# Performance work log

Hardware: AMD Instinct MI355X
Metric: run time of the kernel (lower is better)

Reference implementation:

```python
import jax, jax.numpy as jnp
import numpy as np

NUM_STAGES = 3
EPS = 1e-6


def _l2norm(x, axis):
    return x / (EPS + jnp.linalg.norm(x, axis=axis, keepdims=True))


def _l1norm(x, axis):
    return x / (EPS + jnp.sum(x, axis=axis, keepdims=True))


def setup_inputs() -> dict:
    key = jax.random.key(0)
    k1, k2 = jax.random.split(key)
    B, C, H, W, K = 16, 512, 64, 64, 64
    feats = jax.random.normal(k1, (B, C, H, W), dtype=jnp.float32)
    # bases buffer: N(0, sqrt(2/K)) then l2-normalized along channel dim (done in reference)
    bases = jax.random.normal(k2, (1, C, K), dtype=jnp.float32) * np.sqrt(2.0 / K)
    return {"feats": feats, "bases": bases}


def reference(feats, bases):
    B, C, H, W = feats.shape
    f = feats.reshape(B, C, H * W)              # [B, C, N]
    b = _l2norm(bases, axis=1)                  # match buffer init normalization
    b = jnp.broadcast_to(b, (B, C, b.shape[2])) # [B, C, K]
    attention = None
    for _ in range(NUM_STAGES):
        attention = jnp.einsum('bcn,bck->bnk', f, b)        # [B, N, K]
        attention = jax.nn.softmax(attention, axis=2)
        attention_normed = _l1norm(attention, axis=1)
        b = jnp.einsum('bcn,bnk->bck', f, attention_normed)  # [B, C, K]
        b = _l2norm(b, axis=1)
    # EM loop runs under torch.no_grad in the original
    b = jax.lax.stop_gradient(b)
    attention = jax.lax.stop_gradient(attention)
    feats_recon = jnp.einsum('bck,bnk->bcn', b, attention)   # [B, C, N]
    return feats_recon.reshape(B, C, H, W)
```

## Files before the change

kernel.cpp:

```cpp
#include <hip/hip_runtime.h>
#include <stdint.h>

#define B_ 16
#define C_ 512
#define N_ 4096
#define K_ 64
#define NUM_STAGES 3

typedef __bf16 bf16x8 __attribute__((ext_vector_type(8)));
typedef float f32x4 __attribute__((ext_vector_type(4)));

__device__ __forceinline__ uint16_t f2bf(float x) {
  union { float f; uint32_t u; } v; v.f = x;
  uint32_t r = (v.u + 0x7FFFu + ((v.u >> 16) & 1u)) >> 16;
  return (uint16_t)r;
}

__device__ __forceinline__ void async16(const uint16_t* g, uint16_t* l) {
  __builtin_amdgcn_global_load_lds(
      (const __attribute__((address_space(1))) unsigned int*)g,
      (__attribute__((address_space(3))) unsigned int*)l, 16, 0, 0);
}

__global__ __launch_bounds__(256) void k_prep(const float* __restrict__ feats,
                                              uint16_t* __restrict__ f16,
                                              uint16_t* __restrict__ fT16) {
  __shared__ uint16_t tile[64][65];
  int b = blockIdx.z, c0 = blockIdx.y * 64, n0 = blockIdx.x * 64;
  int t = threadIdx.x;
  const float* src = feats + ((size_t)b * C_ + c0) * N_ + n0;
  uint16_t* dst = f16 + ((size_t)b * C_ + c0) * N_ + n0;
  int cl = t >> 4;
  int nl = (t & 15) * 4;
#pragma unroll
  for (int i = 0; i < 4; ++i) {
    int c = cl + 16 * i;
    float4 v = *(const float4*)(src + (size_t)c * N_ + nl);
    ushort4 x;
    x.x = f2bf(v.x); x.y = f2bf(v.y); x.z = f2bf(v.z); x.w = f2bf(v.w);
    *(ushort4*)(dst + (size_t)c * N_ + nl) = x;
    tile[c][nl + 0] = x.x; tile[c][nl + 1] = x.y;
    tile[c][nl + 2] = x.z; tile[c][nl + 3] = x.w;
  }
  __syncthreads();
  uint16_t* dstT = fT16 + ((size_t)b * N_ + n0) * C_ + c0;
#pragma unroll
  for (int i = 0; i < 4; ++i) {
    int n = cl + 16 * i;
    int c = nl;
    ushort4 y;
    y.x = tile[c + 0][n]; y.y = tile[c + 1][n];
    y.z = tile[c + 2][n]; y.w = tile[c + 3][n];
    *(ushort4*)(dstT + (size_t)n * C_ + c) = y;
  }
}

__global__ __launch_bounds__(256) void k_init_basis(const float* __restrict__ bases,
                                                    uint16_t* __restrict__ basis,
                                                    uint16_t* __restrict__ basisT) {
  int b = blockIdx.x;
  int t = threadIdx.x;
  __shared__ float red[256];
  __shared__ float inv[64];
  int k = t & 63;
  float s = 0.f;
  for (int c = (t >> 6); c < C_; c += 4) {
    float v = bases[c * K_ + k];
    s += v * v;
  }
  red[t] = s;
  __syncthreads();
  if (t < 64) {
    float tot = red[t] + red[t + 64] + red[t + 128] + red[t + 192];
    inv[t] = 1.f / (1e-6f + sqrtf(tot));
  }
  __syncthreads();
  uint16_t* ob = basis + (size_t)b * C_ * K_;
  for (int i = 0; i < (C_ * K_) / 256; ++i) {
    int idx = t + 256 * i;
    int kk = idx & 63;
    ob[idx] = f2bf(bases[idx] * inv[kk]);
  }
  uint16_t* obT = basisT + (size_t)b * K_ * C_;
  for (int i = 0; i < (C_ * K_) / 256; ++i) {
    int idx = t + 256 * i;
    int kk = idx >> 9;
    int cc = idx & 511;
    obT[idx] = f2bf(bases[cc * K_ + kk] * inv[kk]);
  }
}

__global__ __launch_bounds__(512) void k_gemm1(const uint16_t* __restrict__ fT,
                                               const uint16_t* __restrict__ basisT,
                                               uint16_t* __restrict__ attn,
                                               uint16_t* __restrict__ attnT,
                                               int write_attn) {
  extern __shared__ __attribute__((aligned(16))) uint16_t lds[];
  uint16_t* ldsA = lds;
  uint16_t* ldsB = lds + 128 * 256;
  int b = blockIdx.y;
  int n0 = blockIdx.x * 128;
  int t = threadIdx.x;
  int w = t >> 6, lane = t & 63, l15 = lane & 15, quad = lane >> 4;
  const uint16_t* A = fT + ((size_t)b * N_ + n0) * C_;
  const uint16_t* Bm = basisT + (size_t)b * K_ * C_;
  f32x4 acc[4] = {};
  for (int h = 0; h < 2; ++h) {
    int c0h = h * 256;
    __syncthreads();
#pragma unroll
    for (int i = 0; i < 8; ++i) {
      int e = i * 512 + t;
      int row = e >> 5, ch = e & 31;
      async16(A + (size_t)row * C_ + c0h + ((ch + row) & 31) * 8,
              ldsA + (i * 512 + (t & 448)) * 8);
    }
#pragma unroll
    for (int i = 0; i < 4; ++i) {
      int e = i * 512 + t;
      int row = e >> 5, ch = e & 31;
      async16(Bm + (size_t)row * C_ + c0h + ((ch + row) & 31) * 8,
              ldsB + (i * 512 + (t & 448)) * 8);
    }
    __syncthreads();
#pragma unroll
    for (int s = 0; s < 8; ++s) {
      int g = s * 4 + quad;
      int ra = 16 * w + l15;
      bf16x8 af = *(const bf16x8*)(ldsA + ((size_t)ra * 32 + ((g - ra) & 31)) * 8);
#pragma unroll
      for (int kt = 0; kt < 4; ++kt) {
        int rb = 16 * kt + l15;
        bf16x8 bv = *(const bf16x8*)(ldsB + ((size_t)rb * 32 + ((g - rb) & 31)) * 8);
        acc[kt] = __builtin_amdgcn_mfma_f32_16x16x32_bf16(af, bv, acc[kt], 0, 0, 0);
      }
    }
  }
  float p[4][4];
#pragma unroll
  for (int r = 0; r < 4; ++r) {
    float m = fmaxf(fmaxf(acc[0][r], acc[1][r]), fmaxf(acc[2][r], acc[3][r]));
    m = fmaxf(m, __shfl_xor(m, 1));
    m = fmaxf(m, __shfl_xor(m, 2));
    m = fmaxf(m, __shfl_xor(m, 4));
    m = fmaxf(m, __shfl_xor(m, 8));
    float s = 0.f;
#pragma unroll
    for (int kt = 0; kt < 4; ++kt) { p[kt][r] = __expf(acc[kt][r] - m); s += p[kt][r]; }
    s += __shfl_xor(s, 1); s += __shfl_xor(s, 2);
    s += __shfl_xor(s, 4); s += __shfl_xor(s, 8);
    float inv = 1.f / s;
#pragma unroll
    for (int kt = 0; kt < 4; ++kt) p[kt][r] *= inv;
  }
  if (write_attn) {
    uint16_t* oa = attn + ((size_t)b * N_ + n0 + 16 * w + quad * 4) * K_;
#pragma unroll
    for (int r = 0; r < 4; ++r) {
#pragma unroll
      for (int kt = 0; kt < 4; ++kt) oa[(size_t)r * K_ + 16 * kt + l15] = f2bf(p[kt][r]);
    }
  }
#pragma unroll
  for (int kt = 0; kt < 4; ++kt) {
    ushort4 y;
    y.x = f2bf(p[kt][0]); y.y = f2bf(p[kt][1]);
    y.z = f2bf(p[kt][2]); y.w = f2bf(p[kt][3]);
    *(ushort4*)(attnT + ((size_t)b * K_ + 16 * kt + l15) * N_ + n0 + 16 * w + quad * 4) = y;
  }
}

__global__ __launch_bounds__(512) void k_gemm2(const uint16_t* __restrict__ f16,
                                               const uint16_t* __restrict__ attnT,
                                               float* __restrict__ brawT) {
  extern __shared__ __attribute__((aligned(16))) uint16_t lds[];
  uint16_t* ldsF = lds;
  uint16_t* ldsP = lds + 128 * 256;
  int b = blockIdx.z;
  int slice = blockIdx.y;
  int c0 = blockIdx.x * 128;
  int ns0 = slice * 256;
  int t = threadIdx.x;
  int w = t >> 6, lane = t & 63, l15 = lane & 15, quad = lane >> 4;
  const uint16_t* F = f16 + ((size_t)b * C_ + c0) * N_ + ns0;
  const uint16_t* P = attnT + (size_t)b * K_ * N_ + ns0;
#pragma unroll
  for (int i = 0; i < 8; ++i) {
    int e = i * 512 + t;
    int row = e >> 5, ch = e & 31;
    async16(F + (size_t)row * N_ + ((ch + row) & 31) * 8,
            ldsF + (i * 512 + (t & 448)) * 8);
  }
#pragma unroll
  for (int i = 0; i < 4; ++i) {
    int e = i * 512 + t;
    int row = e >> 5, ch = e & 31;
    async16(P + (size_t)row * N_ + ((ch + row) & 31) * 8,
            ldsP + (i * 512 + (t & 448)) * 8);
  }
  f32x4 acc[4] = {};
  __syncthreads();
#pragma unroll
  for (int s = 0; s < 8; ++s) {
    int g = s * 4 + quad;
    int rc = 16 * w + l15;
    bf16x8 fv = *(const bf16x8*)(ldsF + ((size_t)rc * 32 + ((g - rc) & 31)) * 8);
#pragma unroll
    for (int kt = 0; kt < 4; ++kt) {
      int ra = 16 * kt + l15;
      bf16x8 av = *(const bf16x8*)(ldsP + ((size_t)ra * 32 + ((g - ra) & 31)) * 8);
      acc[kt] = __builtin_amdgcn_mfma_f32_16x16x32_bf16(av, fv, acc[kt], 0, 0, 0);
    }
  }
  float* outp = brawT + ((size_t)slice * B_ + b) * K_ * C_;
#pragma unroll
  for (int kt = 0; kt < 4; ++kt) {
#pragma unroll
    for (int r = 0; r < 4; ++r) {
      outp[(size_t)(16 * kt + quad * 4 + r) * C_ + c0 + 16 * w + l15] = acc[kt][r];
    }
  }
}

__global__ __launch_bounds__(256) void k_l2norm(const float* __restrict__ brawT,
                                                uint16_t* __restrict__ basisT,
                                                uint16_t* __restrict__ basis) {
  int b = blockIdx.x, kg = blockIdx.y;
  int t = threadIdx.x, w = t >> 6, lane = t & 63;
  int k = kg * 4 + w;
  float v[8];
#pragma unroll
  for (int j = 0; j < 8; ++j) v[j] = 0.f;
#pragma unroll
  for (int s = 0; s < 16; ++s) {
    const float* rs = brawT + (((size_t)s * B_ + b) * K_ + k) * C_ + lane * 8;
    float4 a = *(const float4*)(rs);
    float4 c4 = *(const float4*)(rs + 4);
    v[0] += a.x; v[1] += a.y; v[2] += a.z; v[3] += a.w;
    v[4] += c4.x; v[5] += c4.y; v[6] += c4.z; v[7] += c4.w;
  }
  float ss = 0.f;
#pragma unroll
  for (int j = 0; j < 8; ++j) ss += v[j] * v[j];
  ss += __shfl_xor(ss, 1); ss += __shfl_xor(ss, 2); ss += __shfl_xor(ss, 4);
  ss += __shfl_xor(ss, 8); ss += __shfl_xor(ss, 16); ss += __shfl_xor(ss, 32);
  float inv = 1.f / (1e-6f + sqrtf(ss));
  uint16_t y[8];
#pragma unroll
  for (int j = 0; j < 8; ++j) y[j] = f2bf(v[j] * inv);
  uint16_t* o = basisT + ((size_t)b * K_ + k) * C_ + lane * 8;
  *(ushort4*)(o) = *(ushort4*)&y[0];
  *(ushort4*)(o + 4) = *(ushort4*)&y[4];
  uint16_t* ob = basis + (size_t)b * C_ * K_ + k;
#pragma unroll
  for (int j = 0; j < 8; ++j) ob[(size_t)(lane * 8 + j) * K_] = y[j];
}

__global__ __launch_bounds__(512) void k_recon(const uint16_t* __restrict__ attn,
                                               const uint16_t* __restrict__ basis,
                                               float* __restrict__ out) {
  __shared__ __attribute__((aligned(16))) uint16_t ldsA[128 * 64];
  __shared__ __attribute__((aligned(16))) uint16_t ldsB[64 * 64];
  int b = blockIdx.z, c0 = blockIdx.y * 64, n0 = blockIdx.x * 128;
  int t = threadIdx.x, w = t >> 6, lane = t & 63, l15 = lane & 15, quad = lane >> 4;
  const uint16_t* A = attn + ((size_t)b * N_ + n0) * K_;
  const uint16_t* Bm = basis + ((size_t)b * C_ + c0) * K_;
#pragma unroll
  for (int r = 0; r < 2; ++r) {
    int e = r * 512 + t;
    int row = e >> 3, ch = e & 7, sch = (ch + row) & 7;
    async16(A + (size_t)row * K_ + sch * 8, ldsA + (r * 512 + (t & 448)) * 8);
  }
  {
    int row = t >> 3, ch = t & 7, sch = (ch + row) & 7;
    async16(Bm + (size_t)row * K_ + sch * 8, ldsB + (t & 448) * 8);
  }
  f32x4 acc[4] = {};
  __syncthreads();
#pragma unroll
  for (int s = 0; s < 2; ++s) {
    int cc = s * 4 + quad;
    int ra = 16 * w + l15;
    bf16x8 af = *(const bf16x8*)(ldsA + (ra * 8 + ((cc - ra) & 7)) * 8);
#pragma unroll
    for (int t4 = 0; t4 < 4; ++t4) {
      int rb = 16 * t4 + l15;
      bf16x8 bv = *(const bf16x8*)(ldsB + (rb * 8 + ((cc - rb) & 7)) * 8);
      acc[t4] = __builtin_amdgcn_mfma_f32_16x16x32_bf16(af, bv, acc[t4], 0, 0, 0);
    }
  }
#pragma unroll
  for (int t4 = 0; t4 < 4; ++t4) {
    int c = c0 + 16 * t4 + l15;
    float4 v = make_float4(acc[t4][0], acc[t4][1], acc[t4][2], acc[t4][3]);
    *(float4*)(out + ((size_t)b * C_ + c) * N_ + n0 + 16 * w + quad * 4) = v;
  }
}

extern "C" void kernel_launch(void* const* d_in, const int* in_sizes, int n_in,
                              void* d_out, int out_size, void* d_ws, size_t ws_size,
                              hipStream_t stream) {
  const float* feats = (const float*)d_in[0];
  const float* bases = (const float*)d_in[1];
  float* out = (float*)d_out;
  char* ws = (char*)d_ws;
  uint16_t* f16 = (uint16_t*)(ws);
  uint16_t* fT16 = (uint16_t*)(ws + 67108864);
  uint16_t* attn = (uint16_t*)(ws + 134217728);
  uint16_t* attnT = (uint16_t*)(ws + 142606336);
  uint16_t* basis = (uint16_t*)(ws + 150994944);
  uint16_t* basisT = (uint16_t*)(ws + 152043520);
  float* brawT = (float*)(ws + 153092096);

  const int ldsBytes = (128 * 256 + 64 * 256) * 2;
  (void)hipFuncSetAttribute((const void*)k_gemm1,
                            hipFuncAttributeMaxDynamicSharedMemorySize, ldsBytes);
  (void)hipFuncSetAttribute((const void*)k_gemm2,
                            hipFuncAttributeMaxDynamicSharedMemorySize, ldsBytes);

  k_prep<<<dim3(64, 8, 16), 256, 0, stream>>>(feats, f16, fT16);
  k_init_basis<<<16, 256, 0, stream>>>(bases, basis, basisT);
  for (int st = 0; st < NUM_STAGES; ++st) {
    k_gemm1<<<dim3(32, 16), 512, ldsBytes, stream>>>(fT16, basisT, attn, attnT,
                                                     st == NUM_STAGES - 1 ? 1 : 0);
    k_gemm2<<<dim3(4, 16, 16), 512, ldsBytes, stream>>>(f16, attnT, brawT);
    k_l2norm<<<dim3(16, 16), 256, 0, stream>>>(brawT, basisT, basis);
  }
  k_recon<<<dim3(32, 8, 16), 512, 0, stream>>>(attn, basis, out);
}
```

Baseline: 491.3 us.

## Retile all kernels to 256-thread blocks with LDS-staged coalesced stores

Every kernel is reworked. k_prep handles 256-column tiles and uses vectorized LDS writes and 16-byte transposed stores. gemm1 and gemm2 move to 256-thread blocks with smaller 64x128 LDS tiles: gemm1 loops over channel chunks, and gemm2 uses fewer split-N slices and writes its partials through LDS in a C-major layout. k_l2norm becomes one 1024-thread block per batch reading that layout. k_recon computes a larger 256x64 tile per block and stages its fp32 output through LDS for coalesced row stores. The aim is better coalescing and fewer partial writes, at the risk of much lower parallelism in the l2norm kernel (16 blocks) and scalar strided basisT stores.

```diff
diff --git a/kernel.cpp b/kernel.cpp
--- a/kernel.cpp
+++ b/kernel.cpp
@@ -25,33 +25,29 @@
 __global__ __launch_bounds__(256) void k_prep(const float* __restrict__ feats,
                                               uint16_t* __restrict__ f16,
                                               uint16_t* __restrict__ fT16) {
-  __shared__ uint16_t tile[64][65];
-  int b = blockIdx.z, c0 = blockIdx.y * 64, n0 = blockIdx.x * 64;
-  int t = threadIdx.x;
+  __shared__ uint16_t tile[64][264];
+  int b = blockIdx.z, c0 = blockIdx.y * 64, n0 = blockIdx.x * 256;
+  int t = threadIdx.x, w = t >> 6, lane = t & 63;
   const float* src = feats + ((size_t)b * C_ + c0) * N_ + n0;
   uint16_t* dst = f16 + ((size_t)b * C_ + c0) * N_ + n0;
-  int cl = t >> 4;
-  int nl = (t & 15) * 4;
-#pragma unroll
-  for (int i = 0; i < 4; ++i) {
-    int c = cl + 16 * i;
-    float4 v = *(const float4*)(src + (size_t)c * N_ + nl);
+  for (int i = 0; i < 16; ++i) {
+    int c = 4 * i + w;
+    int n = lane * 4;
+    float4 v = *(const float4*)(src + (size_t)c * N_ + n);
     ushort4 x;
     x.x = f2bf(v.x); x.y = f2bf(v.y); x.z = f2bf(v.z); x.w = f2bf(v.w);
-    *(ushort4*)(dst + (size_t)c * N_ + nl) = x;
-    tile[c][nl + 0] = x.x; tile[c][nl + 1] = x.y;
-    tile[c][nl + 2] = x.z; tile[c][nl + 3] = x.w;
+    *(ushort4*)(dst + (size_t)c * N_ + n) = x;
+    *(ushort4*)&tile[c][n] = x;
   }
   __syncthreads();
   uint16_t* dstT = fT16 + ((size_t)b * N_ + n0) * C_ + c0;
-#pragma unroll
-  for (int i = 0; i < 4; ++i) {
-    int n = cl + 16 * i;
-    int c = nl;
-    ushort4 y;
-    y.x = tile[c + 0][n]; y.y = tile[c + 1][n];
-    y.z = tile[c + 2][n]; y.w = tile[c + 3][n];
-    *(ushort4*)(dstT + (size_t)n * C_ + c) = y;
+  for (int j = 0; j < 8; ++j) {
+    int n = w * 64 + j * 8 + (lane >> 3);
+    int cb = (lane & 7) * 8;
+    union { uint16_t u[8]; uint4 v; } y;
+#pragma unroll
+    for (int q = 0; q < 8; ++q) y.u[q] = tile[cb + q][n];
+    *(uint4*)(dstT + (size_t)n * C_ + cb) = y.v;
   }
 }
 
@@ -90,48 +86,44 @@
   }
 }
 
-__global__ __launch_bounds__(512) void k_gemm1(const uint16_t* __restrict__ fT,
+__global__ __launch_bounds__(256) void k_gemm1(const uint16_t* __restrict__ fT,
                                                const uint16_t* __restrict__ basisT,
                                                uint16_t* __restrict__ attn,
                                                uint16_t* __restrict__ attnT,
                                                int write_attn) {
-  extern __shared__ __attribute__((aligned(16))) uint16_t lds[];
-  uint16_t* ldsA = lds;
-  uint16_t* ldsB = lds + 128 * 256;
+  __shared__ __attribute__((aligned(16))) uint16_t ldsA[64 * 128];
+  __shared__ __attribute__((aligned(16))) uint16_t ldsB[64 * 128];
   int b = blockIdx.y;
-  int n0 = blockIdx.x * 128;
+  int n0 = blockIdx.x * 64;
   int t = threadIdx.x;
   int w = t >> 6, lane = t & 63, l15 = lane & 15, quad = lane >> 4;
   const uint16_t* A = fT + ((size_t)b * N_ + n0) * C_;
   const uint16_t* Bm = basisT + (size_t)b * K_ * C_;
   f32x4 acc[4] = {};
-  for (int h = 0; h < 2; ++h) {
-    int c0h = h * 256;
+  for (int cs = 0; cs < C_; cs += 128) {
     __syncthreads();
 #pragma unroll
-    for (int i = 0; i < 8; ++i) {
-      int e = i * 512 + t;
-      int row = e >> 5, ch = e & 31;
-      async16(A + (size_t)row * C_ + c0h + ((ch + row) & 31) * 8,
-              ldsA + (i * 512 + (t & 448)) * 8);
-    }
-#pragma unroll
     for (int i = 0; i < 4; ++i) {
-      int e = i * 512 + t;
-      int row = e >> 5, ch = e & 31;
-      async16(Bm + (size_t)row * C_ + c0h + ((ch + row) & 31) * 8,
-              ldsB + (i * 512 + (t & 448)) * 8);
+      int e = i * 256 + t;
+      int row = e >> 4, ch = e & 15, sch = (ch + row) & 15;
+      async16(A + (size_t)row * C_ + cs + sch * 8, ldsA + (i * 256 + (t & 192)) * 8);
+    }
+#pragma unroll
+    for (int i = 0; i < 4; ++i) {
+      int e = i * 256 + t;
+      int row = e >> 4, ch = e & 15, sch = (ch + row) & 15;
+      async16(Bm + (size_t)row * C_ + cs + sch * 8, ldsB + (i * 256 + (t & 192)) * 8);
     }
     __syncthreads();
 #pragma unroll
-    for (int s = 0; s < 8; ++s) {
+    for (int s = 0; s < 4; ++s) {
       int g = s * 4 + quad;
       int ra = 16 * w + l15;
-      bf16x8 af = *(const bf16x8*)(ldsA + ((size_t)ra * 32 + ((g - ra) & 31)) * 8);
+      bf16x8 af = *(const bf16x8*)(ldsA + (ra * 16 + ((g - ra) & 15)) * 8);
 #pragma unroll
       for (int kt = 0; kt < 4; ++kt) {
         int rb = 16 * kt + l15;
-        bf16x8 bv = *(const bf16x8*)(ldsB + ((size_t)rb * 32 + ((g - rb) & 31)) * 8);
+        bf16x8 bv = *(const bf16x8*)(ldsB + (rb * 16 + ((g - rb) & 15)) * 8);
         acc[kt] = __builtin_amdgcn_mfma_f32_16x16x32_bf16(af, bv, acc[kt], 0, 0, 0);
       }
     }
@@ -170,130 +162,162 @@
   }
 }
 
-__global__ __launch_bounds__(512) void k_gemm2(const uint16_t* __restrict__ f16,
+__global__ __launch_bounds__(256) void k_gemm2(const uint16_t* __restrict__ f16,
                                                const uint16_t* __restrict__ attnT,
-                                               float* __restrict__ brawT) {
+                                               float* __restrict__ braw) {
   extern __shared__ __attribute__((aligned(16))) uint16_t lds[];
-  uint16_t* ldsF = lds;
-  uint16_t* ldsP = lds + 128 * 256;
+  uint16_t* ldsP = lds;
+  uint16_t* ldsF = lds + 64 * 128;
   int b = blockIdx.z;
   int slice = blockIdx.y;
-  int c0 = blockIdx.x * 128;
-  int ns0 = slice * 256;
+  int c0 = blockIdx.x * 64;
+  int ns0 = slice * 512;
   int t = threadIdx.x;
   int w = t >> 6, lane = t & 63, l15 = lane & 15, quad = lane >> 4;
-  const uint16_t* F = f16 + ((size_t)b * C_ + c0) * N_ + ns0;
-  const uint16_t* P = attnT + (size_t)b * K_ * N_ + ns0;
-#pragma unroll
-  for (int i = 0; i < 8; ++i) {
-    int e = i * 512 + t;
-    int row = e >> 5, ch = e & 31;
-    async16(F + (size_t)row * N_ + ((ch + row) & 31) * 8,
-            ldsF + (i * 512 + (t & 448)) * 8);
-  }
-#pragma unroll
-  for (int i = 0; i < 4; ++i) {
-    int e = i * 512 + t;
-    int row = e >> 5, ch = e & 31;
-    async16(P + (size_t)row * N_ + ((ch + row) & 31) * 8,
-            ldsP + (i * 512 + (t & 448)) * 8);
-  }
+  const uint16_t* F = f16 + ((size_t)b * C_ + c0) * N_;
+  const uint16_t* P = attnT + (size_t)b * K_ * N_;
   f32x4 acc[4] = {};
-  __syncthreads();
-#pragma unroll
-  for (int s = 0; s < 8; ++s) {
-    int g = s * 4 + quad;
-    int rc = 16 * w + l15;
-    bf16x8 fv = *(const bf16x8*)(ldsF + ((size_t)rc * 32 + ((g - rc) & 31)) * 8);
-#pragma unroll
-    for (int kt = 0; kt < 4; ++kt) {
-      int ra = 16 * kt + l15;
-      bf16x8 av = *(const bf16x8*)(ldsP + ((size_t)ra * 32 + ((g - ra) & 31)) * 8);
-      acc[kt] = __builtin_amdgcn_mfma_f32_16x16x32_bf16(av, fv, acc[kt], 0, 0, 0);
-    }
-  }
-  float* outp = brawT + ((size_t)slice * B_ + b) * K_ * C_;
+  for (int ns = ns0; ns < ns0 + 512; ns += 128) {
+    __syncthreads();
+#pragma unroll
+    for (int i = 0; i < 4; ++i) {
+      int e = i * 256 + t;
+      int row = e >> 4, ch = e & 15, sch = (ch + row) & 15;
+      async16(P + (size_t)row * N_ + ns + sch * 8, ldsP + (i * 256 + (t & 192)) * 8);
+    }
+#pragma unroll
+    for (int i = 0; i < 4; ++i) {
+      int e = i * 256 + t;
+      int row = e >> 4, ch = e & 15, sch = (ch + row) & 15;
+      async16(F + (size_t)row * N_ + ns + sch * 8, ldsF + (i * 256 + (t & 192)) * 8);
+    }
+    __syncthreads();
+#pragma unroll
+    for (int s = 0; s < 4; ++s) {
+      int g = s * 4 + quad;
+      int rc = 16 * w + l15;
+      bf16x8 fv = *(const bf16x8*)(ldsF + (rc * 16 + ((g - rc) & 15)) * 8);
+#pragma unroll
+      for (int kt = 0; kt < 4; ++kt) {
+        int rk = 16 * kt + l15;
+        bf16x8 av = *(const bf16x8*)(ldsP + (rk * 16 + ((g - rk) & 15)) * 8);
+        acc[kt] = __builtin_amdgcn_mfma_f32_16x16x32_bf16(av, fv, acc[kt], 0, 0, 0);
+      }
+    }
+  }
+  __syncthreads();
+  float* ldsT = (float*)lds;
 #pragma unroll
   for (int kt = 0; kt < 4; ++kt) {
-#pragma unroll
-    for (int r = 0; r < 4; ++r) {
-      outp[(size_t)(16 * kt + quad * 4 + r) * C_ + c0 + 16 * w + l15] = acc[kt][r];
-    }
-  }
-}
-
-__global__ __launch_bounds__(256) void k_l2norm(const float* __restrict__ brawT,
-                                                uint16_t* __restrict__ basisT,
-                                                uint16_t* __restrict__ basis) {
-  int b = blockIdx.x, kg = blockIdx.y;
+    float4 v = make_float4(acc[kt][0], acc[kt][1], acc[kt][2], acc[kt][3]);
+    *(float4*)(ldsT + (16 * w + l15) * 68 + 16 * kt + quad * 4) = v;
+  }
+  __syncthreads();
+  float* outp = braw + (((size_t)slice * B_ + b) * C_ + c0) * K_;
+#pragma unroll
+  for (int it = 0; it < 4; ++it) {
+    int c = (t >> 4) + 16 * it;
+    int k = (t & 15) * 4;
+    float4 v = *(const float4*)(ldsT + c * 68 + k);
+    *(float4*)(outp + (size_t)c * K_ + k) = v;
+  }
+}
+
+__global__ __launch_bounds__(1024) void k_l2norm(const float* __restrict__ braw,
+                                                 uint16_t* __restrict__ basisT,
+                                                 uint16_t* __restrict__ basis) {
+  int b = blockIdx.x;
   int t = threadIdx.x, w = t >> 6, lane = t & 63;
-  int k = kg * 4 + w;
-  float v[8];
-#pragma unroll
-  for (int j = 0; j < 8; ++j) v[j] = 0.f;
-#pragma unroll
-  for (int s = 0; s < 16; ++s) {
-    const float* rs = brawT + (((size_t)s * B_ + b) * K_ + k) * C_ + lane * 8;
-    float4 a = *(const float4*)(rs);
-    float4 c4 = *(const float4*)(rs + 4);
-    v[0] += a.x; v[1] += a.y; v[2] += a.z; v[3] += a.w;
-    v[4] += c4.x; v[5] += c4.y; v[6] += c4.z; v[7] += c4.w;
-  }
+  __shared__ float red[16][64];
+  __shared__ float invs[64];
   float ss = 0.f;
-#pragma unroll
-  for (int j = 0; j < 8; ++j) ss += v[j] * v[j];
-  ss += __shfl_xor(ss, 1); ss += __shfl_xor(ss, 2); ss += __shfl_xor(ss, 4);
-  ss += __shfl_xor(ss, 8); ss += __shfl_xor(ss, 16); ss += __shfl_xor(ss, 32);
-  float inv = 1.f / (1e-6f + sqrtf(ss));
-  uint16_t y[8];
-#pragma unroll
-  for (int j = 0; j < 8; ++j) y[j] = f2bf(v[j] * inv);
-  uint16_t* o = basisT + ((size_t)b * K_ + k) * C_ + lane * 8;
-  *(ushort4*)(o) = *(ushort4*)&y[0];
-  *(ushort4*)(o + 4) = *(ushort4*)&y[4];
-  uint16_t* ob = basis + (size_t)b * C_ * K_ + k;
-#pragma unroll
-  for (int j = 0; j < 8; ++j) ob[(size_t)(lane * 8 + j) * K_] = y[j];
-}
-
-__global__ __launch_bounds__(512) void k_recon(const uint16_t* __restrict__ attn,
+  for (int c = w; c < C_; c += 16) {
+    float v = 0.f;
+#pragma unroll
+    for (int s = 0; s < 8; ++s)
+      v += braw[(((size_t)s * B_ + b) * C_ + c) * K_ + lane];
+    ss += v * v;
+  }
+  red[w][lane] = ss;
+  __syncthreads();
+  if (t < 64) {
+    float tot = 0.f;
+#pragma unroll
+    for (int j = 0; j < 16; ++j) tot += red[j][t];
+    invs[t] = 1.f / (1e-6f + sqrtf(tot));
+  }
+  __syncthreads();
+  float inv = invs[lane];
+  for (int c = w; c < C_; c += 16) {
+    float v = 0.f;
+#pragma unroll
+    for (int s = 0; s < 8; ++s)
+      v += braw[(((size_t)s * B_ + b) * C_ + c) * K_ + lane];
+    uint16_t y = f2bf(v * inv);
+    basis[((size_t)b * C_ + c) * K_ + lane] = y;
+    basisT[((size_t)b * K_ + lane) * C_ + c] = y;
+  }
+}
+
+__global__ __launch_bounds__(256) void k_recon(const uint16_t* __restrict__ attn,
                                                const uint16_t* __restrict__ basis,
                                                float* __restrict__ out) {
-  __shared__ __attribute__((aligned(16))) uint16_t ldsA[128 * 64];
-  __shared__ __attribute__((aligned(16))) uint16_t ldsB[64 * 64];
-  int b = blockIdx.z, c0 = blockIdx.y * 64, n0 = blockIdx.x * 128;
+  extern __shared__ __attribute__((aligned(16))) uint16_t lds[];
+  uint16_t* ldsA = lds;
+  uint16_t* ldsB = lds + 256 * 64;
+  int b = blockIdx.z, c0 = blockIdx.y * 64, n0 = blockIdx.x * 256;
   int t = threadIdx.x, w = t >> 6, lane = t & 63, l15 = lane & 15, quad = lane >> 4;
   const uint16_t* A = attn + ((size_t)b * N_ + n0) * K_;
   const uint16_t* Bm = basis + ((size_t)b * C_ + c0) * K_;
 #pragma unroll
-  for (int r = 0; r < 2; ++r) {
-    int e = r * 512 + t;
+  for (int i = 0; i < 8; ++i) {
+    int e = i * 256 + t;
     int row = e >> 3, ch = e & 7, sch = (ch + row) & 7;
-    async16(A + (size_t)row * K_ + sch * 8, ldsA + (r * 512 + (t & 448)) * 8);
-  }
-  {
-    int row = t >> 3, ch = t & 7, sch = (ch + row) & 7;
-    async16(Bm + (size_t)row * K_ + sch * 8, ldsB + (t & 448) * 8);
-  }
-  f32x4 acc[4] = {};
+    async16(A + (size_t)row * K_ + sch * 8, ldsA + (i * 256 + (t & 192)) * 8);
+  }
+#pragma unroll
+  for (int i = 0; i < 2; ++i) {
+    int e = i * 256 + t;
+    int row = e >> 3, ch = e & 7, sch = (ch + row) & 7;
+    async16(Bm + (size_t)row * K_ + sch * 8, ldsB + (i * 256 + (t & 192)) * 8);
+  }
+  f32x4 acc[4][4] = {};
   __syncthreads();
 #pragma unroll
   for (int s = 0; s < 2; ++s) {
-    int cc = s * 4 + quad;
-    int ra = 16 * w + l15;
-    bf16x8 af = *(const bf16x8*)(ldsA + (ra * 8 + ((cc - ra) & 7)) * 8);
-#pragma unroll
-    for (int t4 = 0; t4 < 4; ++t4) {
-      int rb = 16 * t4 + l15;
-      bf16x8 bv = *(const bf16x8*)(ldsB + (rb * 8 + ((cc - rb) & 7)) * 8);
-      acc[t4] = __builtin_amdgcn_mfma_f32_16x16x32_bf16(af, bv, acc[t4], 0, 0, 0);
-    }
-  }
-#pragma unroll
-  for (int t4 = 0; t4 < 4; ++t4) {
-    int c = c0 + 16 * t4 + l15;
-    float4 v = make_float4(acc[t4][0], acc[t4][1], acc[t4][2], acc[t4][3]);
-    *(float4*)(out + ((size_t)b * C_ + c) * N_ + n0 + 16 * w + quad * 4) = v;
+    int g = s * 4 + quad;
+    bf16x8 bv[4];
+#pragma unroll
+    for (int kt = 0; kt < 4; ++kt) {
+      int rb = 16 * kt + l15;
+      bv[kt] = *(const bf16x8*)(ldsB + (rb * 8 + ((g - rb) & 7)) * 8);
+    }
+#pragma unroll
+    for (int mt = 0; mt < 4; ++mt) {
+      int ra = 64 * w + 16 * mt + l15;
+      bf16x8 af = *(const bf16x8*)(ldsA + (ra * 8 + ((g - ra) & 7)) * 8);
+#pragma unroll
+      for (int kt = 0; kt < 4; ++kt)
+        acc[mt][kt] = __builtin_amdgcn_mfma_f32_16x16x32_bf16(af, bv[kt], acc[mt][kt], 0, 0, 0);
+    }
+  }
+  __syncthreads();
+  float* ldsT = (float*)lds;
+#pragma unroll
+  for (int mt = 0; mt < 4; ++mt) {
+#pragma unroll
+    for (int kt = 0; kt < 4; ++kt) {
+      float4 v = make_float4(acc[mt][kt][0], acc[mt][kt][1], acc[mt][kt][2], acc[mt][kt][3]);
+      *(float4*)(ldsT + (16 * kt + l15) * 260 + 64 * w + 16 * mt + quad * 4) = v;
+    }
+  }
+  __syncthreads();
+  float* op = out + ((size_t)b * C_ + c0) * N_ + n0;
+#pragma unroll
+  for (int it = 0; it < 16; ++it) {
+    int c = (t >> 6) + 4 * it;
+    float4 v = *(const float4*)(ldsT + c * 260 + lane * 4);
+    *(float4*)(op + (size_t)c * N_ + lane * 4) = v;
   }
 }
 
@@ -310,21 +334,22 @@
   uint16_t* attnT = (uint16_t*)(ws + 142606336);
   uint16_t* basis = (uint16_t*)(ws + 150994944);
   uint16_t* basisT = (uint16_t*)(ws + 152043520);
-  float* brawT = (float*)(ws + 153092096);
-
-  const int ldsBytes = (128 * 256 + 64 * 256) * 2;
-  (void)hipFuncSetAttribute((const void*)k_gemm1,
-                            hipFuncAttributeMaxDynamicSharedMemorySize, ldsBytes);
+  float* braw = (float*)(ws + 153092096);
+
+  const int ldsG2 = 64 * 128 * 2 * 2;
+  const int ldsRe = 64 * 260 * 4;
   (void)hipFuncSetAttribute((const void*)k_gemm2,
-                            hipFuncAttributeMaxDynamicSharedMemorySize, ldsBytes);
-
-  k_prep<<<dim3(64, 8, 16), 256, 0, stream>>>(feats, f16, fT16);
+                            hipFuncAttributeMaxDynamicSharedMemorySize, ldsG2);
+  (void)hipFuncSetAttribute((const void*)k_recon,
+                            hipFuncAttributeMaxDynamicSharedMemorySize, ldsRe);
+
+  k_prep<<<dim3(16, 8, 16), 256, 0, stream>>>(feats, f16, fT16);
   k_init_basis<<<16, 256, 0, stream>>>(bases, basis, basisT);
   for (int st = 0; st < NUM_STAGES; ++st) {
-    k_gemm1<<<dim3(32, 16), 512, ldsBytes, stream>>>(fT16, basisT, attn, attnT,
-                                                     st == NUM_STAGES - 1 ? 1 : 0);
-    k_gemm2<<<dim3(4, 16, 16), 512, ldsBytes, stream>>>(f16, attnT, brawT);
-    k_l2norm<<<dim3(16, 16), 256, 0, stream>>>(brawT, basisT, basis);
-  }
-  k_recon<<<dim3(32, 8, 16), 512, 0, stream>>>(attn, basis, out);
-}
+    k_gemm1<<<dim3(64, 16), 256, 0, stream>>>(fT16, basisT, attn, attnT,
+                                              st == NUM_STAGES - 1 ? 1 : 0);
+    k_gemm2<<<dim3(8, 8, 16), 256, ldsG2, stream>>>(f16, attnT, braw);
+    k_l2norm<<<16, 1024, 0, stream>>>(braw, basisT, basis);
+  }
+  k_recon<<<dim3(16, 8, 16), 256, ldsRe, stream>>>(attn, basis, out);
+}
```

Result: slower. 627.8 us (+27.8%).
